# Performance work log

Hardware: AMD Instinct MI355X
Metric: run time of the kernel (lower is better)

The kernel has to match this reference:

```python
import jax, jax.numpy as jnp
import numpy as np

DEPTH_CHANNEL = 48  # max_disp(192) / downsample_scale(4)


def setup_inputs() -> dict:
    key = jax.random.key(0)
    k1, k2 = jax.random.split(key)
    B, C, H, W = 4, 512, 96, 312
    left_features = jax.random.normal(k1, (B, C, H, W), dtype=jnp.float32)
    right_features = jax.random.normal(k2, (B, C, H, W), dtype=jnp.float32)
    return {"left_features": left_features, "right_features": right_features}


def reference(left_features, right_features):
    # PSM cosine cost volume: for each disparity i,
    #   cost[:, i, :, i:] = mean_c(left[:, :, :, i:] * right[:, :, :, :W-i])
    # positions w < i remain zero (from the pre-zeroed tensor in the original).
    B, C, H, W = left_features.shape
    planes = []
    for i in range(DEPTH_CHANNEL):  # small fixed disparity loop (48), unrolled under jit
        corr = jnp.mean(
            left_features[:, :, :, i:] * right_features[:, :, :, : W - i],
            axis=1,
        )  # [B, H, W-i]
        planes.append(jnp.pad(corr, ((0, 0), (0, 0), (i, 0))))  # zero-fill w < i
    return jnp.stack(planes, axis=1)  # [B, D, H, W]
```

## Files before the change

### kernel.cpp

```cpp
#include <hip/hip_runtime.h>
#include <hip/hip_bf16.h>
#include <stdint.h>


#define B_ 4
#define C_ 512
#define H_ 96
#define W_ 312
#define D_ 48
#define HW_ (H_ * W_)
#define CHW_ (C_ * HW_)

#define KC 64
#define NCHUNK (C_ / KC)
#define NQ 4
#define QW 80
#define LCOLS 80
#define RCOLS 128
#define PITCH 128
#define LBYTES (LCOLS * PITCH)
#define RBYTES (RCOLS * PITCH)
#define SMEM_HALF (LBYTES + RBYTES)
#define SMEM_BYTES (2 * SMEM_HALF)

#define THREADS 256
#define NWG (NQ * H_ * B_)
#define LITEMS 3
#define RITEMS 4

typedef __bf16 bf16x8 __attribute__((ext_vector_type(8)));
typedef float  f32x4  __attribute__((ext_vector_type(4)));

__device__ __forceinline__ uint32_t pack2_bf16(float a, float b) {
    uint32_t r;
    asm("v_cvt_pk_bf16_f32 %0, %1, %2" : "=v"(r) : "v"(a), "v"(b));
    return r;
}

__device__ __forceinline__ int lds_slotoff(int lw, int chi) {
    return lw * PITCH + ((chi ^ (lw & 7) ^ ((lw >> 4) & 7)) << 4);
}

__device__ __forceinline__ void lds_barrier() {
    asm volatile("s_waitcnt lgkmcnt(0)" ::: "memory");
    __builtin_amdgcn_s_barrier();
}

__global__ __launch_bounds__(THREADS, 2)
void psm_cost_volume(const float* __restrict__ lf,
                     const float* __restrict__ rf,
                     float* __restrict__ out) {
    const int lid = blockIdx.x;
    const int swz = (lid & 7) * (NWG / 8) + (lid >> 3);
    const int q   = swz & 3;
    const int t   = swz >> 2;
    const int b   = t / H_;
    const int h   = t - b * H_;
    const int wq  = q * QW;

    const int tid  = threadIdx.x;
    const int lane = tid & 63;
    const int wave = tid >> 6;
    const int l15  = lane & 15;
    const int l4   = lane >> 4;
    const int jj   = wave;

    extern __shared__ char smem[];

    const float* lbase = lf + (size_t)b * CHW_ + (size_t)h * W_;
    const float* rbase = rf + (size_t)b * CHW_ + (size_t)h * W_;

    f32x4 acc[5];
    #pragma unroll
    for (int i = 0; i < 5; ++i) acc[i] = f32x4{0.f, 0.f, 0.f, 0.f};

    f32x4 pl0[LITEMS], pl1[LITEMS], pr0[RITEMS], pr1[RITEMS];

    auto LOADS = [&](int c0) {
        #pragma unroll
        for (int it = 0; it < LITEMS; ++it) {
            int idx = tid + it * THREADS;
            if (idx < 32 * 20) {
                int rp = idx / 20;
                int q4 = idx - rp * 20;
                int w4 = wq + 4 * q4;
                pl0[it] = f32x4{0.f, 0.f, 0.f, 0.f};
                pl1[it] = f32x4{0.f, 0.f, 0.f, 0.f};
                if (w4 + 3 < W_) {
                    const float* g = lbase + (size_t)(c0 + 2 * rp) * HW_ + w4;
                    pl0[it] = *(const f32x4*)g;
                    pl1[it] = *(const f32x4*)(g + HW_);
                }
            }
        }
        #pragma unroll
        for (int it = 0; it < RITEMS; ++it) {
            int idx = tid + it * THREADS;
            int rp  = idx >> 5;
            int q4  = idx & 31;
            int w4  = wq - 48 + 4 * q4;
            pr0[it] = f32x4{0.f, 0.f, 0.f, 0.f};
            pr1[it] = f32x4{0.f, 0.f, 0.f, 0.f};
            if (w4 >= 0 && w4 + 3 < W_) {
                const float* g = rbase + (size_t)(c0 + 2 * rp) * HW_ + w4;
                pr0[it] = *(const f32x4*)g;
                pr1[it] = *(const f32x4*)(g + HW_);
            }
        }
    };

    auto WRITES = [&](char* buf) {
        #pragma unroll
        for (int it = 0; it < LITEMS; ++it) {
            int idx = tid + it * THREADS;
            if (idx < 32 * 20) {
                int rp  = idx / 20;
                int q4  = idx - rp * 20;
                int chi = rp >> 2;
                int cb  = (rp & 3) << 2;
                #pragma unroll
                for (int j = 0; j < 4; ++j) {
                    int lw = 4 * q4 + j;
                    *(uint32_t*)(buf + lds_slotoff(lw, chi) + cb) =
                        pack2_bf16(pl0[it][j], pl1[it][j]);
                }
            }
        }
        #pragma unroll
        for (int it = 0; it < RITEMS; ++it) {
            int idx = tid + it * THREADS;
            int rp  = idx >> 5;
            int q4  = idx & 31;
            int chi = rp >> 2;
            int cb  = (rp & 3) << 2;
            #pragma unroll
            for (int j = 0; j < 4; ++j) {
                int lw = 4 * q4 + j;
                *(uint32_t*)(buf + LBYTES + lds_slotoff(lw, chi) + cb) =
                    pack2_bf16(pr0[it][j], pr1[it][j]);
            }
        }
    };

    LOADS(0);
    WRITES(smem);
    LOADS(KC);
    lds_barrier();

    for (int ch = 0; ch < NCHUNK; ++ch) {
        const int cur = ch & 1;
        const char* rdbuf = smem + cur * SMEM_HALF;

        #pragma unroll
        for (int ks = 0; ks < 2; ++ks) {
            const int chi = ks * 4 + l4;
            #pragma unroll
            for (int pi = 0; pi < 5; ++pi) {
                const int lwB = 16 * pi + l15;
                const int lwA = 16 * (pi + jj) + l15;
                bf16x8 bfrag = *(const bf16x8*)(rdbuf + lds_slotoff(lwB, chi));
                bf16x8 afrag = *(const bf16x8*)(rdbuf + LBYTES + lds_slotoff(lwA, chi));
                acc[pi] = __builtin_amdgcn_mfma_f32_16x16x32_bf16(afrag, bfrag, acc[pi], 0, 0, 0);
            }
        }

        if (ch + 1 < NCHUNK) {
            WRITES(smem + (cur ^ 1) * SMEM_HALF);
            if (ch + 2 < NCHUNK) LOADS((ch + 2) * KC);
            lds_barrier();
        }
    }
    __syncthreads();

    float* outs = (float*)smem;
    #pragma unroll
    for (int pi = 0; pi < 5; ++pi) {
        const int lw = 16 * pi + l15;
        #pragma unroll
        for (int r = 0; r < 4; ++r) {
            int tm = 4 * l4 + r;
            int d  = 48 - 16 * jj + l15 - tm;
            if (d >= 0 && d < D_) {
                outs[d * QW + lw] = acc[pi][r] * (1.f / 512.f);
            }
        }
    }
    __syncthreads();

    float* obase = out + (size_t)b * (D_ * HW_) + (size_t)h * W_ + wq;
    #pragma unroll
    for (int it = 0; it < (D_ * QW) / THREADS; ++it) {
        int idx = it * THREADS + tid;
        int d   = idx / QW;
        int lw  = idx - d * QW;
        if (wq + lw < W_) {
            obase[(size_t)d * HW_ + lw] = outs[idx];
        }
    }
}

extern "C" void kernel_launch(void* const* d_in, const int* in_sizes, int n_in,
                              void* d_out, int out_size, void* d_ws, size_t ws_size,
                              hipStream_t stream) {
    const float* lf = (const float*)d_in[0];
    const float* rf = (const float*)d_in[1];
    float* out = (float*)d_out;
    psm_cost_volume<<<dim3(NWG), THREADS, SMEM_BYTES, stream>>>(lf, rf, out);
}
```

Measured before the change: 111.9 us.

## Shrink channel chunk to 32 and single-buffer LDS to raise occupancy

Halves the channel chunk per iteration and drops LDS double buffering to a single buffer with an 80-byte pitch and a new 4-slot XOR swizzle. Register prefetch arrays shrink, and the launch attribute now asks for 6 waves per EU instead of 2 blocks, aiming for more resident waves to hide global load latency. In exchange there are twice as many chunk iterations, each with two barriers, and only register-level prefetch overlaps compute with the next load.

```diff
diff --git a/kernel.cpp b/kernel.cpp
--- a/kernel.cpp
+++ b/kernel.cpp
@@ -11,22 +11,21 @@
 #define HW_ (H_ * W_)
 #define CHW_ (C_ * HW_)
 
-#define KC 64
+#define KC 32
 #define NCHUNK (C_ / KC)
 #define NQ 4
 #define QW 80
 #define LCOLS 80
 #define RCOLS 128
-#define PITCH 128
+#define PITCH 80
 #define LBYTES (LCOLS * PITCH)
 #define RBYTES (RCOLS * PITCH)
-#define SMEM_HALF (LBYTES + RBYTES)
-#define SMEM_BYTES (2 * SMEM_HALF)
+#define SMEM_BYTES (LBYTES + RBYTES)
 
 #define THREADS 256
 #define NWG (NQ * H_ * B_)
-#define LITEMS 3
-#define RITEMS 4
+#define LITEMS 2
+#define RITEMS 2
 
 typedef __bf16 bf16x8 __attribute__((ext_vector_type(8)));
 typedef float  f32x4  __attribute__((ext_vector_type(4)));
@@ -38,7 +37,8 @@
 }
 
 __device__ __forceinline__ int lds_slotoff(int lw, int chi) {
-    return lw * PITCH + ((chi ^ (lw & 7) ^ ((lw >> 4) & 7)) << 4);
+    int s = (chi ^ (lw & 3) ^ ((lw >> 2) & 3) ^ ((lw >> 4) & 3)) & 3;
+    return lw * PITCH + (s << 4);
 }
 
 __device__ __forceinline__ void lds_barrier() {
@@ -46,7 +46,8 @@
     __builtin_amdgcn_s_barrier();
 }
 
-__global__ __launch_bounds__(THREADS, 2)
+__global__ __launch_bounds__(THREADS)
+__attribute__((amdgpu_waves_per_eu(6)))
 void psm_cost_volume(const float* __restrict__ lf,
                      const float* __restrict__ rf,
                      float* __restrict__ out) {
@@ -80,7 +81,7 @@
         #pragma unroll
         for (int it = 0; it < LITEMS; ++it) {
             int idx = tid + it * THREADS;
-            if (idx < 32 * 20) {
+            if (idx < 16 * 20) {
                 int rp = idx / 20;
                 int q4 = idx - rp * 20;
                 int w4 = wq + 4 * q4;
@@ -109,11 +110,11 @@
         }
     };
 
-    auto WRITES = [&](char* buf) {
+    auto WRITES = [&]() {
         #pragma unroll
         for (int it = 0; it < LITEMS; ++it) {
             int idx = tid + it * THREADS;
-            if (idx < 32 * 20) {
+            if (idx < 16 * 20) {
                 int rp  = idx / 20;
                 int q4  = idx - rp * 20;
                 int chi = rp >> 2;
@@ -121,7 +122,7 @@
                 #pragma unroll
                 for (int j = 0; j < 4; ++j) {
                     int lw = 4 * q4 + j;
-                    *(uint32_t*)(buf + lds_slotoff(lw, chi) + cb) =
+                    *(uint32_t*)(smem + lds_slotoff(lw, chi) + cb) =
                         pack2_bf16(pl0[it][j], pl1[it][j]);
                 }
             }
@@ -136,38 +137,26 @@
             #pragma unroll
             for (int j = 0; j < 4; ++j) {
                 int lw = 4 * q4 + j;
-                *(uint32_t*)(buf + LBYTES + lds_slotoff(lw, chi) + cb) =
+                *(uint32_t*)(smem + LBYTES + lds_slotoff(lw, chi) + cb) =
                     pack2_bf16(pr0[it][j], pr1[it][j]);
             }
         }
     };
 
     LOADS(0);
-    WRITES(smem);
-    LOADS(KC);
-    lds_barrier();
-
     for (int ch = 0; ch < NCHUNK; ++ch) {
-        const int cur = ch & 1;
-        const char* rdbuf = smem + cur * SMEM_HALF;
+        if (ch) lds_barrier();
+        WRITES();
+        if (ch + 1 < NCHUNK) LOADS((ch + 1) * KC);
+        lds_barrier();
 
         #pragma unroll
-        for (int ks = 0; ks < 2; ++ks) {
-            const int chi = ks * 4 + l4;
-            #pragma unroll
-            for (int pi = 0; pi < 5; ++pi) {
-                const int lwB = 16 * pi + l15;
-                const int lwA = 16 * (pi + jj) + l15;
-                bf16x8 bfrag = *(const bf16x8*)(rdbuf + lds_slotoff(lwB, chi));
-                bf16x8 afrag = *(const bf16x8*)(rdbuf + LBYTES + lds_slotoff(lwA, chi));
-                acc[pi] = __builtin_amdgcn_mfma_f32_16x16x32_bf16(afrag, bfrag, acc[pi], 0, 0, 0);
-            }
-        }
-
-        if (ch + 1 < NCHUNK) {
-            WRITES(smem + (cur ^ 1) * SMEM_HALF);
-            if (ch + 2 < NCHUNK) LOADS((ch + 2) * KC);
-            lds_barrier();
+        for (int pi = 0; pi < 5; ++pi) {
+            const int lwB = 16 * pi + l15;
+            const int lwA = 16 * (pi + jj) + l15;
+            bf16x8 bfrag = *(const bf16x8*)(smem + lds_slotoff(lwB, l4));
+            bf16x8 afrag = *(const bf16x8*)(smem + LBYTES + lds_slotoff(lwA, l4));
+            acc[pi] = __builtin_amdgcn_mfma_f32_16x16x32_bf16(afrag, bfrag, acc[pi], 0, 0, 0);
         }
     }
     __syncthreads();
```

After: 176.4 us. 57.6% more time.
